# Performance work log

Hardware: AMD Instinct MI355X
Metric: run time of the kernel (lower is better)

## Reference

```python
import jax, jax.numpy as jnp
import numpy as np

INPUT_DIM = 1024
OUTPUT_DIM = 1000
DEPTH = 10
LAMBDA_REG = 1e-3
N_INTERNAL = 2 ** DEPTH - 1
N_LEAF = 2 ** DEPTH
BATCH = 16384


def setup_inputs() -> dict:
    key = jax.random.key(0)
    k1, k2, k3 = jax.random.split(key, 3)
    X = jax.random.normal(k1, (BATCH, INPUT_DIM), dtype=jnp.float32)
    # torch nn.Linear weight layout: [out_features, in_features]; scaled to keep
    # sigmoid routing probs away from 0/1 saturation (log-reg term).
    W_internal = jax.random.normal(k2, (N_INTERNAL, INPUT_DIM + 1), dtype=jnp.float32) * 0.02
    W_leaf = jax.random.normal(k3, (OUTPUT_DIM, N_LEAF), dtype=jnp.float32) * 0.02
    return {"X": X, "W_internal": W_internal, "W_leaf": W_leaf}


def _tree_paths(X, W_internal):
    B = X.shape[0]
    Xb = jnp.concatenate([jnp.ones((B, 1), X.dtype), X], axis=1)  # [B, D+1]
    logits = jax.nn.sigmoid(Xb @ W_internal.T)                    # [B, N_int]
    routing = jnp.stack([logits, 1.0 - logits], axis=2)           # [B, N_int, 2]
    path = jnp.ones((B, 1), X.dtype)
    reg = jnp.float32(0.0)
    start = 0
    for layer in range(DEPTH):
        n = 2 ** layer
        lp = routing[:, start:start + n, :].reshape(B, 2 * n)     # next_paths [B, 2n]
        path = jnp.repeat(path, 2, axis=1) * lp                   # new path probs [B, 2n]
        # Faithful to source: parent_idx = node_idx // 2 indexes the UPDATED path probs.
        parent = jnp.repeat(path[:, :n], 2, axis=1)               # [B, 2n]
        num = jnp.sum(lp * parent, axis=0)                        # [2n]
        den = jnp.sum(parent, axis=0) + 1e-8                      # [2n]
        alpha = num / den
        factor = LAMBDA_REG * 2.0 ** (-layer)
        reg = reg + factor * jnp.sum(-0.5 * (jnp.log(alpha) + jnp.log(1.0 - alpha)))
        start += n
    return path, reg  # path: [B, 2^DEPTH]


def reference(X, W_internal, W_leaf):
    path_probs, reg = _tree_paths(X, W_internal)
    predictions = path_probs @ W_leaf.T   # [B, output_dim]
    return predictions, reg
```

## Files before the change

### kernel.cpp

```cpp
#include <hip/hip_runtime.h>
#include <hip/hip_bf16.h>

#define B_ROWS 16384
#define K_DIM  1024
#define N_INT  1023
#define N_OUT  1000

using s8vec = __attribute__((ext_vector_type(8))) short;
using f32x4 = __attribute__((ext_vector_type(4))) float;

static const size_t OFF_XB   = 0;
static const size_t OFF_W1   = OFF_XB   + 33554432;
static const size_t OFF_BIAS = OFF_W1   + 2097152;
static const size_t OFF_PROB = OFF_BIAS + 4096;
static const size_t OFF_PATH = OFF_PROB + 33554432;
static const size_t OFF_W2   = OFF_PATH + 33554432;
static const size_t OFF_SG   = OFF_W2   + 2097152;

__device__ __forceinline__ float b2f(ushort u) {
  return __uint_as_float(((unsigned)u) << 16);
}
__device__ __forceinline__ float blo(unsigned u) { return __uint_as_float(u << 16); }
__device__ __forceinline__ float bhi(unsigned u) { return __uint_as_float(u & 0xffff0000u); }
__device__ __forceinline__ ushort f2b(float f) {
  unsigned u = __float_as_uint(f);
  u = u + 0x7FFFu + ((u >> 16) & 1u);
  return (ushort)(u >> 16);
}

__device__ __forceinline__ void load_lds16(const ushort* g, ushort* l) {
  __builtin_amdgcn_global_load_lds((const __attribute__((address_space(1))) void*)g,
                                   (__attribute__((address_space(3))) void*)l,
                                   16, 0, 0);
}

__global__ __launch_bounds__(256) void cvt_x(const float4* __restrict__ X,
                                             ushort4* __restrict__ O) {
  const int i = blockIdx.x * 256 + threadIdx.x;
  const float4 v = X[i];
  ushort4 o;
  o.x = f2b(v.x); o.y = f2b(v.y); o.z = f2b(v.z); o.w = f2b(v.w);
  O[i] = o;
}

__global__ __launch_bounds__(256) void cvt_w(const float* __restrict__ Wi,
                                             const float* __restrict__ Wl,
                                             ushort* __restrict__ W1,
                                             ushort* __restrict__ W2,
                                             float* __restrict__ bias) {
  const int idx = blockIdx.x * 256 + threadIdx.x;
  if (idx < (1 << 20)) {
    const int n = idx >> 10, k = idx & 1023;
    const float v = (n < N_INT) ? Wi[n * 1025 + 1 + k] : 0.f;
    W1[idx] = f2b(v);
    if (k == 0) bias[n] = (n < N_INT) ? Wi[n * 1025] : 0.f;
  } else {
    const int j = idx - (1 << 20);
    const int n = j >> 10, k = j & 1023;
    const float v = (n < N_OUT) ? Wl[n * 1024 + k] : 0.f;
    W2[j] = f2b(v);
  }
}

template <int MODE>
__global__ __launch_bounds__(256, 4) void gemm_bt(const ushort* __restrict__ A,
                                                  const ushort* __restrict__ Bm,
                                                  const float* __restrict__ bias,
                                                  void* __restrict__ outp) {
  __shared__ ushort As[4096];
  __shared__ ushort Bs[4096];
  const int tid = threadIdx.x;
  const int bm = blockIdx.x, bn = blockIdx.y;
  const int lane = tid & 63, wv = tid >> 6;
  const int wm = wv >> 1, wn = wv & 1;
  const int m16 = lane & 15, q = lane >> 4;
  const int qs = q ^ ((m16 >> 1) & 3);

  const int r0 = tid >> 2;
  const int qsw = (tid & 3) ^ ((r0 >> 1) & 3);
  const ushort* aG = A  + (size_t)(bm * 128 + r0) * 1024 + qsw * 8;
  const ushort* bG = Bm + (size_t)(bn * 128 + r0) * 1024 + qsw * 8;
  ushort* AsW = As + wv * 512;
  ushort* BsW = Bs + wv * 512;

  f32x4 acc[4][4] = {};

  for (int k0 = 0; k0 < 1024; k0 += 32) {
    if (k0) __syncthreads();
    load_lds16(aG + k0, AsW);
    load_lds16(aG + 65536 + k0, AsW + 2048);
    load_lds16(bG + k0, BsW);
    load_lds16(bG + 65536 + k0, BsW + 2048);
    __syncthreads();

    s8vec af[4], bfv[4];
#pragma unroll
    for (int i = 0; i < 4; ++i)
      af[i] = *(const s8vec*)(As + (wm * 64 + i * 16 + m16) * 32 + qs * 8);
#pragma unroll
    for (int j = 0; j < 4; ++j)
      bfv[j] = *(const s8vec*)(Bs + (wn * 64 + j * 16 + m16) * 32 + qs * 8);
#pragma unroll
    for (int i = 0; i < 4; ++i)
#pragma unroll
      for (int j = 0; j < 4; ++j)
        acc[i][j] = __builtin_amdgcn_mfma_f32_16x16x32_bf16(af[i], bfv[j], acc[i][j], 0, 0, 0);
  }

  if (MODE == 0) {
    ushort* P = (ushort*)outp;
#pragma unroll
    for (int i = 0; i < 4; ++i)
#pragma unroll
      for (int r = 0; r < 4; ++r) {
        const int gr = bm * 128 + wm * 64 + i * 16 + q * 4 + r;
#pragma unroll
        for (int j = 0; j < 4; ++j) {
          const int gc = bn * 128 + wn * 64 + j * 16 + m16;
          const float z = acc[i][j][r] + bias[gc];
          const float p = 1.f / (1.f + expf(-z));
          if (gc < N_INT) P[(size_t)gr * 1024 + gc + 1] = f2b(p);
        }
      }
  } else {
    float* O = (float*)outp;
#pragma unroll
    for (int i = 0; i < 4; ++i)
#pragma unroll
      for (int r = 0; r < 4; ++r) {
        const int gr = bm * 128 + wm * 64 + i * 16 + q * 4 + r;
#pragma unroll
        for (int j = 0; j < 4; ++j) {
          const int gc = bn * 128 + wn * 64 + j * 16 + m16;
          if (gc < N_OUT) O[(size_t)gr * 1000 + gc] = acc[i][j][r];
        }
      }
  }
}

__global__ __launch_bounds__(256) void tree_kernel(const ushort* __restrict__ probs,
                                                   ushort* __restrict__ path,
                                                   float* __restrict__ Sg) {
  __shared__ float Ss[4096];
  for (int i = threadIdx.x; i < 4096; i += 256) Ss[i] = 0.f;
  __syncthreads();
  const int lane = threadIdx.x & 63;
  const int gw = blockIdx.x * 4 + (threadIdx.x >> 6);

  float at1[6] = {}, at2[6] = {};
  float ae1[30] = {}, ae2[30] = {};

  ushort h4[4], p6a[4]; uint p7a[4]; uint2 p8a[4]; uint4 p9a[4];
#pragma unroll
  for (int rr = 0; rr < 4; ++rr) {
    const ushort* prow = probs + (size_t)(gw * 4 + rr) * 1024;
    h4[rr]  = prow[lane];
    p6a[rr] = prow[64 + lane];
    p7a[rr] = *(const uint*)(prow + 128 + 2 * lane);
    p8a[rr] = *(const uint2*)(prow + 256 + 4 * lane);
    p9a[rr] = *(const uint4*)(prow + 512 + 8 * lane);
  }

#pragma unroll
  for (int rr = 0; rr < 4; ++rr) {
    const int r = gw * 4 + rr;
    const int hh = (int)h4[rr];
    const ushort p6 = p6a[rr];
    const uint   p7 = p7a[rr];
    const uint2  p8 = p8a[rr];
    const uint4  p9 = p9a[rr];

    float v = 1.f;
#pragma unroll
    for (int t = 1; t <= 6; ++t) {
      const int ell = t - 1;
      const int e = lane >> (6 - t);
      const float p = b2f((ushort)__shfl(hh, (1 << ell) + (e >> 1)));
      v *= (e & 1) ? (1.f - p) : p;
      const float pj = b2f((ushort)__shfl(hh, ((1 << ell) + e) & 63));
      if (((lane & ((1 << (6 - t)) - 1)) == 0) && (e < (1 << ell))) {
        at1[ell] += v;
        at2[ell] += pj * v;
      }
    }

    float w[16];
    {
      const float p = b2f(p6);
      w[1] = v * (1.f - p); w[0] = v * p;
    }
    {
      const int j0 = __shfl((int)p6, 2 * lane);
      const int j1 = __shfl((int)p6, 2 * lane + 1);
      if (lane < 32) {
        ae1[0] += w[0]; ae2[0] += b2f((ushort)j0) * w[0];
        ae1[1] += w[1]; ae2[1] += b2f((ushort)j1) * w[1];
      }
    }
    {
      const float pA = blo(p7), pB = bhi(p7);
      w[3] = w[1] * (1.f - pB); w[2] = w[1] * pB;
      w[1] = w[0] * (1.f - pA); w[0] = w[0] * pA;
    }
    {
      const uint ua = (uint)__shfl((int)p7, 2 * lane);
      const uint ub = (uint)__shfl((int)p7, 2 * lane + 1);
      if (lane < 32) {
        ae1[2] += w[0]; ae2[2] += blo(ua) * w[0];
        ae1[3] += w[1]; ae2[3] += bhi(ua) * w[1];
        ae1[4] += w[2]; ae2[4] += blo(ub) * w[2];
        ae1[5] += w[3]; ae2[5] += bhi(ub) * w[3];
      }
    }
    {
      const float pv[4] = { blo(p8.x), bhi(p8.x), blo(p8.y), bhi(p8.y) };
#pragma unroll
      for (int i = 3; i >= 0; --i) {
        w[2 * i + 1] = w[i] * (1.f - pv[i]);
        w[2 * i]     = w[i] * pv[i];
      }
    }
    {
      const uint u0 = (uint)__shfl((int)p8.x, 2 * lane);
      const uint u1 = (uint)__shfl((int)p8.y, 2 * lane);
      const uint u2 = (uint)__shfl((int)p8.x, 2 * lane + 1);
      const uint u3 = (uint)__shfl((int)p8.y, 2 * lane + 1);
      if (lane < 32) {
        ae1[6]  += w[0]; ae2[6]  += blo(u0) * w[0];
        ae1[7]  += w[1]; ae2[7]  += bhi(u0) * w[1];
        ae1[8]  += w[2]; ae2[8]  += blo(u1) * w[2];
        ae1[9]  += w[3]; ae2[9]  += bhi(u1) * w[3];
        ae1[10] += w[4]; ae2[10] += blo(u2) * w[4];
        ae1[11] += w[5]; ae2[11] += bhi(u2) * w[5];
        ae1[12] += w[6]; ae2[12] += blo(u3) * w[6];
        ae1[13] += w[7]; ae2[13] += bhi(u3) * w[7];
      }
    }
    {
      const uint pv[4] = { p9.x, p9.y, p9.z, p9.w };
#pragma unroll
      for (int i = 7; i >= 0; --i) {
        const float p = (i & 1) ? bhi(pv[i >> 1]) : blo(pv[i >> 1]);
        w[2 * i + 1] = w[i] * (1.f - p);
        w[2 * i]     = w[i] * p;
      }
    }
    {
      uint s_[8];
      s_[0] = (uint)__shfl((int)p9.x, 2 * lane);
      s_[1] = (uint)__shfl((int)p9.y, 2 * lane);
      s_[2] = (uint)__shfl((int)p9.z, 2 * lane);
      s_[3] = (uint)__shfl((int)p9.w, 2 * lane);
      s_[4] = (uint)__shfl((int)p9.x, 2 * lane + 1);
      s_[5] = (uint)__shfl((int)p9.y, 2 * lane + 1);
      s_[6] = (uint)__shfl((int)p9.z, 2 * lane + 1);
      s_[7] = (uint)__shfl((int)p9.w, 2 * lane + 1);
      if (lane < 32) {
#pragma unroll
        for (int i = 0; i < 16; ++i) {
          const uint u = s_[i >> 1];
          const float pj = (i & 1) ? bhi(u) : blo(u);
          ae1[14 + i] += w[i]; ae2[14 + i] += pj * w[i];
        }
      }
    }
    union { ushort u[16]; uint4 q4[2]; } pk;
#pragma unroll
    for (int i = 0; i < 16; ++i) pk.u[i] = f2b(w[i]);
    uint4* dst = (uint4*)(path + (size_t)r * 1024 + lane * 16);
    dst[0] = pk.q4[0];
    dst[1] = pk.q4[1];
  }

#pragma unroll
  for (int t = 1; t <= 6; ++t) {
    const int ell = t - 1;
    const int e = lane >> (6 - t);
    if (((lane & ((1 << (6 - t)) - 1)) == 0) && (e < (1 << ell))) {
      const int node = (1 << ell) - 1 + e;
      atomicAdd(&Ss[node], at1[ell]);
      atomicAdd(&Ss[2048 + node], at2[ell]);
    }
  }
  if (lane < 32) {
#pragma unroll
    for (int ell = 6; ell <= 9; ++ell) {
      const int s = 1 << (ell - 6);
      const int pb = (1 << ell) - 1;
      const int base = 2 * s - 2;
#pragma unroll
      for (int i = 0; i < 2 * s; ++i) {
        const int node = pb + 2 * s * lane + i;
        atomicAdd(&Ss[node], ae1[base + i]);
        atomicAdd(&Ss[2048 + node], ae2[base + i]);
      }
    }
  }
  __syncthreads();
  for (int i = threadIdx.x; i < 1023; i += 256) {
    atomicAdd(&Sg[i], Ss[i]);
    atomicAdd(&Sg[2048 + i], Ss[2048 + i]);
  }
}

__global__ __launch_bounds__(1024) void finalize_kernel(const float* __restrict__ Sg,
                                                        float* __restrict__ outreg) {
  const int tid = threadIdx.x;
  double val = 0.0;
  if (tid < 1023) {
    const int ell = 31 - __clz(tid + 1);
    const double s1 = (double)Sg[tid];
    const double s2 = (double)Sg[2048 + tid];
    const double den = s1 + 1e-8;
    const double a0 = s2 / den;
    const double a1 = (s1 - s2) / den;
    const double f = 1e-3 * (1.0 / (double)(1 << ell));
    val = -0.5 * f * (log(a0) + log(1.0 - a0) + log(a1) + log(1.0 - a1));
  }
#pragma unroll
  for (int o = 32; o > 0; o >>= 1) val += __shfl_down(val, o, 64);
  __shared__ double partd[16];
  if ((tid & 63) == 0) partd[tid >> 6] = val;
  __syncthreads();
  if (tid == 0) {
    double t = 0.0;
    for (int i = 0; i < 16; ++i) t += partd[i];
    outreg[0] = (float)t;
  }
}

extern "C" void kernel_launch(void* const* d_in, const int* in_sizes, int n_in,
                              void* d_out, int out_size, void* d_ws, size_t ws_size,
                              hipStream_t stream) {
  const float* X     = (const float*)d_in[0];
  const float* Wint  = (const float*)d_in[1];
  const float* Wleaf = (const float*)d_in[2];
  float* out = (float*)d_out;
  char* ws = (char*)d_ws;

  ushort* Xb   = (ushort*)(ws + OFF_XB);
  ushort* W1   = (ushort*)(ws + OFF_W1);
  float*  bias = (float*)(ws + OFF_BIAS);
  ushort* prob = (ushort*)(ws + OFF_PROB);
  ushort* path = (ushort*)(ws + OFF_PATH);
  ushort* W2   = (ushort*)(ws + OFF_W2);
  float*  Sg   = (float*)(ws + OFF_SG);

  (void)hipMemsetAsync(ws + OFF_SG, 0, 16384, stream);
  cvt_x<<<16384, 256, 0, stream>>>((const float4*)X, (ushort4*)Xb);
  cvt_w<<<8192, 256, 0, stream>>>(Wint, Wleaf, W1, W2, bias);
  gemm_bt<0><<<dim3(128, 8), 256, 0, stream>>>(Xb, W1, bias, (void*)prob);
  tree_kernel<<<1024, 256, 0, stream>>>(prob, path, Sg);
  gemm_bt<1><<<dim3(128, 8), 256, 0, stream>>>(path, W2, nullptr, (void*)out);
  finalize_kernel<<<1, 1024, 0, stream>>>(Sg, out + (size_t)B_ROWS * N_OUT);
}
```

Before: 306.0 us.

## Replace global tree-stat atomics with per-block partials and a reduce kernel

Each tree_kernel block now writes its 2046 per-node sums to its own slice of a partial buffer instead of issuing global atomicAdds. A new 32-block reduce kernel sums 64 partials each before doing far fewer atomics. The tree kernel also handles 2 rows per wave over twice as many blocks, and the two conversion kernels are merged into one launch. The partial buffer reuses the probability workspace that tree_kernel is still reading. A block can overwrite rows another block has not read yet, so this is a race risk.

```diff
diff --git a/kernel.cpp b/kernel.cpp
--- a/kernel.cpp
+++ b/kernel.cpp
@@ -34,31 +34,33 @@
                                    16, 0, 0);
 }
 
-__global__ __launch_bounds__(256) void cvt_x(const float4* __restrict__ X,
-                                             ushort4* __restrict__ O) {
-  const int i = blockIdx.x * 256 + threadIdx.x;
-  const float4 v = X[i];
-  ushort4 o;
-  o.x = f2b(v.x); o.y = f2b(v.y); o.z = f2b(v.z); o.w = f2b(v.w);
-  O[i] = o;
-}
-
-__global__ __launch_bounds__(256) void cvt_w(const float* __restrict__ Wi,
-                                             const float* __restrict__ Wl,
-                                             ushort* __restrict__ W1,
-                                             ushort* __restrict__ W2,
-                                             float* __restrict__ bias) {
-  const int idx = blockIdx.x * 256 + threadIdx.x;
-  if (idx < (1 << 20)) {
-    const int n = idx >> 10, k = idx & 1023;
-    const float v = (n < N_INT) ? Wi[n * 1025 + 1 + k] : 0.f;
-    W1[idx] = f2b(v);
-    if (k == 0) bias[n] = (n < N_INT) ? Wi[n * 1025] : 0.f;
+__global__ __launch_bounds__(256) void cvt_all(const float4* __restrict__ X,
+                                               ushort4* __restrict__ O,
+                                               const float* __restrict__ Wi,
+                                               const float* __restrict__ Wl,
+                                               ushort* __restrict__ W1,
+                                               ushort* __restrict__ W2,
+                                               float* __restrict__ bias) {
+  const int b = blockIdx.x;
+  if (b < 16384) {
+    const int i = b * 256 + threadIdx.x;
+    const float4 v = X[i];
+    ushort4 o;
+    o.x = f2b(v.x); o.y = f2b(v.y); o.z = f2b(v.z); o.w = f2b(v.w);
+    O[i] = o;
   } else {
-    const int j = idx - (1 << 20);
-    const int n = j >> 10, k = j & 1023;
-    const float v = (n < N_OUT) ? Wl[n * 1024 + k] : 0.f;
-    W2[j] = f2b(v);
+    const int idx = (b - 16384) * 256 + threadIdx.x;
+    if (idx < (1 << 20)) {
+      const int n = idx >> 10, k = idx & 1023;
+      const float v = (n < N_INT) ? Wi[n * 1025 + 1 + k] : 0.f;
+      W1[idx] = f2b(v);
+      if (k == 0) bias[n] = (n < N_INT) ? Wi[n * 1025] : 0.f;
+    } else {
+      const int j = idx - (1 << 20);
+      const int n = j >> 10, k = j & 1023;
+      const float v = (n < N_OUT) ? Wl[n * 1024 + k] : 0.f;
+      W2[j] = f2b(v);
+    }
   }
 }
 
@@ -140,7 +142,7 @@
 
 __global__ __launch_bounds__(256) void tree_kernel(const ushort* __restrict__ probs,
                                                    ushort* __restrict__ path,
-                                                   float* __restrict__ Sg) {
+                                                   float* __restrict__ Spart) {
   __shared__ float Ss[4096];
   for (int i = threadIdx.x; i < 4096; i += 256) Ss[i] = 0.f;
   __syncthreads();
@@ -150,10 +152,10 @@
   float at1[6] = {}, at2[6] = {};
   float ae1[30] = {}, ae2[30] = {};
 
-  ushort h4[4], p6a[4]; uint p7a[4]; uint2 p8a[4]; uint4 p9a[4];
-#pragma unroll
-  for (int rr = 0; rr < 4; ++rr) {
-    const ushort* prow = probs + (size_t)(gw * 4 + rr) * 1024;
+  ushort h4[2], p6a[2]; uint p7a[2]; uint2 p8a[2]; uint4 p9a[2];
+#pragma unroll
+  for (int rr = 0; rr < 2; ++rr) {
+    const ushort* prow = probs + (size_t)(gw * 2 + rr) * 1024;
     h4[rr]  = prow[lane];
     p6a[rr] = prow[64 + lane];
     p7a[rr] = *(const uint*)(prow + 128 + 2 * lane);
@@ -162,8 +164,8 @@
   }
 
 #pragma unroll
-  for (int rr = 0; rr < 4; ++rr) {
-    const int r = gw * 4 + rr;
+  for (int rr = 0; rr < 2; ++rr) {
+    const int r = gw * 2 + rr;
     const int hh = (int)h4[rr];
     const ushort p6 = p6a[rr];
     const uint   p7 = p7a[rr];
@@ -297,9 +299,28 @@
     }
   }
   __syncthreads();
-  for (int i = threadIdx.x; i < 1023; i += 256) {
-    atomicAdd(&Sg[i], Ss[i]);
-    atomicAdd(&Sg[2048 + i], Ss[2048 + i]);
+  float* Sp = Spart + (size_t)blockIdx.x * 2048;
+  for (int i = threadIdx.x; i < 2048; i += 256) {
+    const int node = i & 1023;
+    Sp[i] = (i < 1024) ? Ss[node] : Ss[2048 + node];
+  }
+}
+
+__global__ __launch_bounds__(256) void reduce_kernel(const float* __restrict__ Spart,
+                                                     float* __restrict__ Sg) {
+  const int t = threadIdx.x;
+  float acc[8] = {};
+  const float* base = Spart + (size_t)blockIdx.x * 64 * 2048;
+  for (int b = 0; b < 64; ++b) {
+    const float* p = base + (size_t)b * 2048;
+#pragma unroll
+    for (int k = 0; k < 8; ++k) acc[k] += p[t + 256 * k];
+  }
+#pragma unroll
+  for (int k = 0; k < 8; ++k) {
+    const int i = t + 256 * k;
+    const int node = i & 1023;
+    if (node < 1023) atomicAdd(&Sg[(i < 1024 ? 0 : 2048) + node], acc[k]);
   }
 }
 
@@ -345,12 +366,14 @@
   ushort* path = (ushort*)(ws + OFF_PATH);
   ushort* W2   = (ushort*)(ws + OFF_W2);
   float*  Sg   = (float*)(ws + OFF_SG);
+  float*  Spart = (float*)(ws + OFF_PROB);
 
   (void)hipMemsetAsync(ws + OFF_SG, 0, 16384, stream);
-  cvt_x<<<16384, 256, 0, stream>>>((const float4*)X, (ushort4*)Xb);
-  cvt_w<<<8192, 256, 0, stream>>>(Wint, Wleaf, W1, W2, bias);
+  cvt_all<<<24576, 256, 0, stream>>>((const float4*)X, (ushort4*)Xb,
+                                     Wint, Wleaf, W1, W2, bias);
   gemm_bt<0><<<dim3(128, 8), 256, 0, stream>>>(Xb, W1, bias, (void*)prob);
-  tree_kernel<<<1024, 256, 0, stream>>>(prob, path, Sg);
+  tree_kernel<<<2048, 256, 0, stream>>>(prob, path, Spart);
   gemm_bt<1><<<dim3(128, 8), 256, 0, stream>>>(path, W2, nullptr, (void*)out);
+  reduce_kernel<<<32, 256, 0, stream>>>(Spart, Sg);
   finalize_kernel<<<1, 1024, 0, stream>>>(Sg, out + (size_t)B_ROWS * N_OUT);
 }
```

New measurement: 344.0 us. +12.4%, slower.
